# Kernel tuning notes

Hardware: AMD Instinct MI355X
Metric: run time of the kernel (lower is better)

## Reference

```python
import jax, jax.numpy as jnp
import numpy as np

N_NODES = 20000
N_EDGES = 600000
HID = 128
HEADS = 4
NUM_IN = 2 * HID
N_BATCH = 64


def _gelu(x):
    return jax.nn.gelu(x, approximate=False)


def _bn(x, g, b, eps=1e-5):
    # BatchNorm1d, training-mode math: biased variance over the batch dim
    m = jnp.mean(x, axis=0)
    v = jnp.var(x, axis=0)
    return g * (x - m) * jax.lax.rsqrt(v + eps) + b


def setup_inputs() -> dict:
    keys = iter(jax.random.split(jax.random.key(0), 64))

    def nk():
        return next(keys)

    def lin(i, o):
        return (jax.random.normal(nk(), (i, o), jnp.float32) / np.sqrt(i)).astype(jnp.float32)

    def zeros(o):
        return jnp.zeros((o,), jnp.float32)

    inp = {
        "h_V": jax.random.normal(nk(), (N_NODES, HID), jnp.float32),
        "h_E": jax.random.normal(nk(), (N_EDGES, HID), jnp.float32),
        "edge_idx": jax.random.randint(nk(), (2, N_EDGES), 0, N_NODES),
        "batch_id": jnp.sort(jax.random.randint(nk(), (N_NODES,), 0, N_BATCH)),
        # NeighborAttention.W_V (num_in -> hid -> hid -> hid)
        "wv1_w": lin(NUM_IN, HID), "wv1_b": zeros(HID),
        "wv2_w": lin(HID, HID), "wv2_b": zeros(HID),
        "wv3_w": lin(HID, HID), "wv3_b": zeros(HID),
        # NeighborAttention.Bias (3*hid -> hid -> hid -> heads)
        "bb1_w": lin(3 * HID, HID), "bb1_b": zeros(HID),
        "bb2_w": lin(HID, HID), "bb2_b": zeros(HID),
        "bb3_w": lin(HID, HEADS), "bb3_b": zeros(HEADS),
        # NeighborAttention.W_O (no bias)
        "wo_w": lin(HID, HID),
        # GeneralGNN norms 0 and 1
        "n0_g": jnp.ones((HID,), jnp.float32), "n0_b": zeros(HID),
        "n1_g": jnp.ones((HID,), jnp.float32), "n1_b": zeros(HID),
        # dense FFN (hid -> 4*hid -> hid)
        "d1_w": lin(HID, 4 * HID), "d1_b": zeros(4 * HID),
        "d2_w": lin(4 * HID, HID), "d2_b": zeros(HID),
        # EdgeMLP (3*hid -> hid -> hid -> hid) + its norm
        "e1_w": lin(3 * HID, HID), "e1_b": zeros(HID),
        "e2_w": lin(HID, HID), "e2_b": zeros(HID),
        "e3_w": lin(HID, HID), "e3_b": zeros(HID),
        "en_g": jnp.ones((HID,), jnp.float32), "en_b": zeros(HID),
    }
    return inp


def _forward(h_V, h_E, src, dst,
             wv1_w, wv1_b, wv2_w, wv2_b, wv3_w, wv3_b,
             bb1_w, bb1_b, bb2_w, bb2_b, bb3_w, bb3_b,
             wo_w, n0_g, n0_b, n1_g, n1_b,
             d1_w, d1_b, d2_w, d2_b,
             e1_w, e1_b, e2_w, e2_b, e3_w, e3_b, en_g, en_b):
    N = h_V.shape[0]
    d_head = HID // HEADS
    # attention input: cat([h_E, h_V[dst]]) with center_id = src
    h_E_in = jnp.concatenate([h_E, h_V[dst]], axis=-1)  # (E, 2*HID)
    x = jnp.concatenate([h_V[src], h_E_in], axis=-1)     # (E, 3*HID)
    # Bias MLP -> per-edge per-head logits; the sqrt(d) * 1/sqrt(d) scaling cancels
    w = _gelu(x @ bb1_w + bb1_b)
    w = _gelu(w @ bb2_w + bb2_b)
    w = w @ bb3_w + bb3_b                                 # (E, HEADS)
    # value MLP
    V = _gelu(h_E_in @ wv1_w + wv1_b)
    V = _gelu(V @ wv2_w + wv2_b)
    V = (V @ wv3_w + wv3_b).reshape(-1, HEADS, d_head)    # (E, HEADS, d)
    # scatter_softmax over edges sharing a source node
    m = jax.ops.segment_max(w, src, num_segments=N)
    m = jnp.where(jnp.isfinite(m), m, 0.0)
    ew = jnp.exp(w - m[src])
    denom = jax.ops.segment_sum(ew, src, num_segments=N)
    attend = ew / denom[src]                              # (E, HEADS)
    agg = jax.ops.segment_sum(attend[:, :, None] * V, src, num_segments=N)
    dh = agg.reshape(N, HID) @ wo_w                       # W_O
    h_V = _bn(h_V + dh, n0_g, n0_b)
    dh = _gelu(h_V @ d1_w + d1_b) @ d2_w + d2_b           # dense FFN
    h_V = _bn(h_V + dh, n1_g, n1_b)
    # EdgeMLP update
    h_EV = jnp.concatenate([h_V[src], h_E, h_V[dst]], axis=-1)
    msg = _gelu(h_EV @ e1_w + e1_b)
    msg = _gelu(msg @ e2_w + e2_b)
    msg = msg @ e3_w + e3_b
    h_E = _bn(h_E + msg, en_g, en_b)
    # Context with node_context=edge_context=0 is identity
    return (h_V, h_E)


def reference(h_V, h_E, edge_idx, batch_id,
              wv1_w, wv1_b, wv2_w, wv2_b, wv3_w, wv3_b,
              bb1_w, bb1_b, bb2_w, bb2_b, bb3_w, bb3_b,
              wo_w, n0_g, n0_b, n1_g, n1_b,
              d1_w, d1_b, d2_w, d2_b,
              e1_w, e1_b, e2_w, e2_b, e3_w, e3_b, en_g, en_b):
    src, dst = edge_idx[0], edge_idx[1]
    return _forward(h_V, h_E, src, dst,
                    wv1_w, wv1_b, wv2_w, wv2_b, wv3_w, wv3_b,
                    bb1_w, bb1_b, bb2_w, bb2_b, bb3_w, bb3_b,
                    wo_w, n0_g, n0_b, n1_g, n1_b,
                    d1_w, d1_b, d2_w, d2_b,
                    e1_w, e1_b, e2_w, e2_b, e3_w, e3_b, en_g, en_b)
```

## Files before the change

kernel.cpp:

```cpp
#include <hip/hip_runtime.h>
#include <cstdint>
#include <cstddef>

#define NN 20000
#define NE 600000

typedef unsigned short u16;
typedef unsigned int   u32;
typedef __bf16 bf16x8 __attribute__((ext_vector_type(8)));
typedef float  f32x4  __attribute__((ext_vector_type(4)));

constexpr int PK_BB1 = 0;
constexpr int PK_BB2 = PK_BB1 + 384 * 128;
constexpr int PK_WV1 = PK_BB2 + 128 * 128;
constexpr int PK_WV2 = PK_WV1 + 256 * 128;
constexpr int PK_WV3 = PK_WV2 + 128 * 128;
constexpr int PK_WO  = PK_WV3 + 128 * 128;
constexpr int PK_D1  = PK_WO  + 128 * 128;
constexpr int PK_D2  = PK_D1  + 128 * 512;
constexpr int PK_E1  = PK_D2  + 512 * 128;
constexpr int PK_E2  = PK_E1  + 384 * 128;
constexpr int PK_E3  = PK_E2  + 128 * 128;
constexpr int PK_BB3 = PK_E3  + 128 * 128;

constexpr size_t WS_PW    = 0;
constexpr size_t WS_STATS = 0x100000;
constexpr size_t WS_FLAG  = WS_STATS + 3072;
constexpr size_t WS_HIST  = WS_STATS + 0x1000;
constexpr size_t WS_OFFS  = WS_HIST + 0x14000;
constexpr size_t WS_CNT   = WS_OFFS + 0x14000;
constexpr size_t WS_EIDS  = WS_CNT + 0x14000;
constexpr size_t WS_WLOG  = WS_EIDS + 0x250000;
constexpr size_t WS_AGG   = WS_WLOG + 0x930000;
constexpr size_t WS_R     = WS_AGG + 0xA00000;

__device__ __forceinline__ float bf2f(u16 u) {
    return __builtin_bit_cast(float, (u32)u << 16);
}
__device__ __forceinline__ u16 f2bf(float f) {
    u32 x = __builtin_bit_cast(u32, f);
    return (u16)((x + 0x7FFFu + ((x >> 16) & 1u)) >> 16);
}
__device__ __forceinline__ float gelu_f(float x) {
    float z = fabsf(x) * 0.70710678118654752f;
    float t = 1.0f / fmaf(0.3275911f, z, 1.0f);
    float p = t * fmaf(t, fmaf(t, fmaf(t, fmaf(t, 1.061405429f, -1.453152027f),
                                       1.421413741f), -0.284496736f), 0.254829592f);
    float erfz = fmaf(-p, __expf(-z * z), 1.0f);
    float u = 0.5f * x;
    return fmaf(copysignf(erfz, x), u, u);
}
__device__ __forceinline__ float ldv(const void* p, size_t i, int m) {
    return m ? ((const float*)p)[i] : bf2f(((const u16*)p)[i]);
}
#define MFMA(a, b, c) __builtin_amdgcn_mfma_f32_16x16x32_bf16(a, b, c, 0, 0, 0)

#define TM 32
#define XS 136

__device__ __forceinline__ void mma128(const u16* __restrict__ xl, const u16* __restrict__ wp,
                                       int kcBase, int nDiv16, int wave, int lane,
                                       f32x4 acc[2][2]) {
#pragma unroll
    for (int kc = 0; kc < 4; ++kc) {
        int koff = kc * 32 + (lane >> 4) * 8;
        bf16x8 a0 = *(const bf16x8*)&xl[((lane & 15)) * XS + koff];
        bf16x8 a1 = *(const bf16x8*)&xl[((lane & 15) + 16) * XS + koff];
#pragma unroll
        for (int ni = 0; ni < 2; ++ni) {
            int nc = wave * 2 + ni;
            bf16x8 b = *(const bf16x8*)&wp[(((size_t)(kcBase + kc) * nDiv16 + nc) * 64 + lane) * 8];
            acc[0][ni] = MFMA(a0, b, acc[0][ni]);
            acc[1][ni] = MFMA(a1, b, acc[1][ni]);
        }
    }
}

__device__ __forceinline__ void epi_lds(f32x4 acc[2][2], u16* hl, const void* biasG,
                                        int wave, int lane, bool doGelu, int f32m) {
    int col0 = wave * 32;
#pragma unroll
    for (int ni = 0; ni < 2; ++ni) {
        int col = col0 + ni * 16 + (lane & 15);
        float b = ldv(biasG, col, f32m);
#pragma unroll
        for (int mi = 0; mi < 2; ++mi) {
            int rb = mi * 16 + (lane >> 4) * 4;
#pragma unroll
            for (int r = 0; r < 4; ++r) {
                float v = acc[mi][ni][r] + b;
                if (doGelu) v = gelu_f(v);
                hl[(rb + r) * XS + col] = f2bf(v);
            }
        }
    }
}

__device__ __forceinline__ void stage_row8(u16* dst8, const void* table, size_t row, int c8, int f32m) {
    if (f32m) {
        const float* s = (const float*)table + row * 128 + c8 * 8;
        float4 v0 = *(const float4*)s;
        float4 v1 = *(const float4*)(s + 4);
        uint4 o;
        o.x = (u32)f2bf(v0.x) | ((u32)f2bf(v0.y) << 16);
        o.y = (u32)f2bf(v0.z) | ((u32)f2bf(v0.w) << 16);
        o.z = (u32)f2bf(v1.x) | ((u32)f2bf(v1.y) << 16);
        o.w = (u32)f2bf(v1.z) | ((u32)f2bf(v1.w) << 16);
        *(uint4*)dst8 = o;
    } else {
        *(uint4*)dst8 = *(const uint4*)((const u16*)table + row * 128 + c8 * 8);
    }
}

__device__ __forceinline__ void stage_idx(u16* dst, const void* table, const int* idx, int tid, int f32m) {
    int r0 = tid >> 4, c = tid & 15;
#pragma unroll
    for (int p = 0; p < 2; ++p) {
        int r = r0 + p * 16;
        stage_row8(&dst[r * XS + c * 8], table, (size_t)idx[r], c, f32m);
    }
}
__device__ __forceinline__ void stage_seq(u16* dst, const void* table, size_t rowBase, int tid, int f32m) {
    int r0 = tid >> 4, c = tid & 15;
#pragma unroll
    for (int p = 0; p < 2; ++p) {
        int r = r0 + p * 16;
        stage_row8(&dst[r * XS + c * 8], table, rowBase + r, c, f32m);
    }
}

__global__ void k_detect(const void* hV, int* flag) {
    int l = threadIdx.x;
    const u16* p = (const u16*)hV;
    float m = fmaxf(fabsf(bf2f(p[l])), fabsf(bf2f(p[64 + l])));
    for (int s = 1; s < 64; s <<= 1) m = fmaxf(m, __shfl_xor(m, s));
    if (l == 0) *flag = (m > 1e4f) ? 1 : 0;
}

__global__ void k_pack(const void* bb1, const void* bb2, const void* wv1, const void* wv2,
                       const void* wv3, const void* wo, const void* d1, const void* d2,
                       const void* e1, const void* e2, const void* e3, const void* bb3,
                       u16* pw, const int* dflag) {
    int f32m = *dflag;
    const int Ks[12] = {384, 128, 256, 128, 128, 128, 128, 512, 384, 128, 128, 128};
    const int Ns[12] = {128, 128, 128, 128, 128, 128, 512, 128, 128, 128, 128, 16};
    const void* srcs[12] = {bb1, bb2, wv1, wv2, wv3, wo, d1, d2, e1, e2, e3, bb3};
    int gid = blockIdx.x * 256 + threadIdx.x;
    int lane = gid & 63;
    int fid = gid >> 6;
    if (fid >= 708) return;
    int w = 0, base = 0, dstoff = 0;
    for (int i = 0; i < 12; ++i) {
        int nf = (Ks[i] / 32) * (Ns[i] / 16);
        if (fid < base + nf) { w = i; break; }
        base += nf;
        dstoff += Ks[i] * Ns[i];
    }
    int f = fid - base;
    int N = Ns[w];
    int kc = f / (N / 16), nc = f % (N / 16);
    const void* S = srcs[w];
    u16* D = pw + dstoff + ((size_t)f * 64 + lane) * 8;
    int krow = kc * 32 + (lane >> 4) * 8;
    int col = nc * 16 + (lane & 15);
#pragma unroll
    for (int j = 0; j < 8; ++j) {
        float v;
        if (w == 11) v = (col < 4) ? ldv(S, (size_t)(krow + j) * 4 + col, f32m) : 0.f;
        else         v = ldv(S, (size_t)(krow + j) * N + col, f32m);
        D[j] = f2bf(v);
    }
}

__global__ void k_hist(const int* src, int* hist) {
    int e = blockIdx.x * 256 + threadIdx.x;
    if (e < NE) atomicAdd(&hist[src[e]], 1);
}

__global__ void k_scan(const int* hist, int* offs, int* cnt) {
    __shared__ int buf[1024];
    __shared__ int carry;
    if (threadIdx.x == 0) carry = 0;
    __syncthreads();
    for (int b = 0; b < NN; b += 1024) {
        int i = b + threadIdx.x;
        int v = (i < NN) ? hist[i] : 0;
        buf[threadIdx.x] = v;
        __syncthreads();
        for (int s = 1; s < 1024; s <<= 1) {
            int t = (threadIdx.x >= s) ? buf[threadIdx.x - s] : 0;
            __syncthreads();
            buf[threadIdx.x] += t;
            __syncthreads();
        }
        int excl = buf[threadIdx.x] - v + carry;
        if (i < NN) { offs[i] = excl; cnt[i] = excl; }
        __syncthreads();
        if (threadIdx.x == 1023) carry += buf[1023];
        __syncthreads();
    }
    if (threadIdx.x == 0) offs[NN] = carry;
}

__global__ void k_fill(const int* src, int* cnt, int* eids) {
    int e = blockIdx.x * 256 + threadIdx.x;
    if (e < NE) {
        int slot = atomicAdd(&cnt[src[e]], 1);
        eids[slot] = e;
    }
}

__global__ __launch_bounds__(256, 2) void k_edge1(
    const void* __restrict__ hV, const void* __restrict__ hE, const int* __restrict__ eidx,
    const u16* __restrict__ pw, const void* bb1b, const void* bb2b,
    const void* bb3b, const void* wv1b, const void* wv2b, const void* wv3b,
    float* __restrict__ wlog, void* __restrict__ dout, const int* dflag) {
    __shared__ __attribute__((aligned(16))) u16 xb[TM * XS];
    __shared__ __attribute__((aligned(16))) u16 h1b[TM * XS];
    __shared__ __attribute__((aligned(16))) u16 h1v[TM * XS];
    __shared__ int sIdx[TM], dIdx[TM];
    int f32m = *dflag;
    int tid = threadIdx.x, wave = tid >> 6, lane = tid & 63;
    long e0 = (long)blockIdx.x * TM;
    if (tid < TM) {
        sIdx[tid] = eidx[e0 + tid];
        dIdx[tid] = eidx[NE + e0 + tid];
    }
    __syncthreads();

    f32x4 accB[2][2] = {};
    f32x4 accV[2][2] = {};
    stage_idx(xb, hV, sIdx, tid, f32m);
    __syncthreads();
    mma128(xb, pw + PK_BB1, 0, 8, wave, lane, accB);
    __syncthreads();
    stage_seq(xb, hE, (size_t)e0, tid, f32m);
    __syncthreads();
    mma128(xb, pw + PK_BB1, 4, 8, wave, lane, accB);
    mma128(xb, pw + PK_WV1, 0, 8, wave, lane, accV);
    __syncthreads();
    stage_idx(xb, hV, dIdx, tid, f32m);
    __syncthreads();
    mma128(xb, pw + PK_BB1, 8, 8, wave, lane, accB);
    mma128(xb, pw + PK_WV1, 4, 8, wave, lane, accV);
    __syncthreads();
    epi_lds(accB, h1b, bb1b, wave, lane, true, f32m);
    epi_lds(accV, h1v, wv1b, wave, lane, true, f32m);
    __syncthreads();
    f32x4 accB2[2][2] = {};
    f32x4 accV2[2][2] = {};
    mma128(h1b, pw + PK_BB2, 0, 8, wave, lane, accB2);
    mma128(h1v, pw + PK_WV2, 0, 8, wave, lane, accV2);
    __syncthreads();
    epi_lds(accB2, xb, bb2b, wave, lane, true, f32m);
    epi_lds(accV2, h1b, wv2b, wave, lane, true, f32m);
    __syncthreads();
    u16* Vout = (u16*)((char*)dout + (size_t)NN * 128 * (f32m ? 4 : 2));
    f32x4 accV3[2][2] = {};
    mma128(h1b, pw + PK_WV3, 0, 8, wave, lane, accV3);
    {
        int col0 = wave * 32;
#pragma unroll
        for (int ni = 0; ni < 2; ++ni) {
            int col = col0 + ni * 16 + (lane & 15);
            float b = ldv(wv3b, col, f32m);
#pragma unroll
            for (int mi = 0; mi < 2; ++mi) {
                int rb = mi * 16 + (lane >> 4) * 4;
#pragma unroll
                for (int r = 0; r < 4; ++r) {
                    long row = e0 + rb + r;
                    Vout[row * 128 + col] = f2bf(accV3[mi][ni][r] + b);
                }
            }
        }
    }
    if (wave == 0) {
        f32x4 aw0 = {0.f, 0.f, 0.f, 0.f};
        f32x4 aw1 = {0.f, 0.f, 0.f, 0.f};
#pragma unroll
        for (int kc = 0; kc < 4; ++kc) {
            int koff = kc * 32 + (lane >> 4) * 8;
            bf16x8 a0 = *(const bf16x8*)&xb[(lane & 15) * XS + koff];
            bf16x8 a1 = *(const bf16x8*)&xb[((lane & 15) + 16) * XS + koff];
            bf16x8 b = *(const bf16x8*)&pw[PK_BB3 + ((size_t)kc * 64 + lane) * 8];
            aw0 = MFMA(a0, b, aw0);
            aw1 = MFMA(a1, b, aw1);
        }
        if ((lane & 15) < 4) {
            int col = lane & 15;
            int rbase = (lane >> 4) * 4;
            float b3 = ldv(bb3b, col, f32m);
#pragma unroll
            for (int r = 0; r < 4; ++r) {
                wlog[(e0 + rbase + r) * 4 + col] = aw0[r] + b3;
                wlog[(e0 + 16 + rbase + r) * 4 + col] = aw1[r] + b3;
            }
        }
    }
}

__global__ void k_agg(const int* __restrict__ offs, const int* __restrict__ eids,
                      const float* __restrict__ wlog, const void* __restrict__ dout,
                      float* __restrict__ agg, const int* dflag) {
    int f32m = *dflag;
    const u16* V = (const u16*)((const char*)dout + (size_t)NN * 128 * (f32m ? 4 : 2));
    int node = blockIdx.x;
    int l = threadIdx.x;
    int beg = offs[node], end = offs[node + 1];
    int deg = end - beg;
    if (deg == 0) {
        agg[(size_t)node * 128 + 2 * l] = 0.f;
        agg[(size_t)node * 128 + 2 * l + 1] = 0.f;
        return;
    }
    int h = l & 3;
    float lmax = -3.0e38f;
    for (int i = (l >> 2); i < deg; i += 16) {
        int e = eids[beg + i];
        lmax = fmaxf(lmax, wlog[(size_t)e * 4 + h]);
    }
    for (int s = 4; s < 64; s <<= 1) lmax = fmaxf(lmax, __shfl_xor(lmax, s));
    float lsum = 0.f;
    for (int i = (l >> 2); i < deg; i += 16) {
        int e = eids[beg + i];
        lsum += __expf(wlog[(size_t)e * 4 + h] - lmax);
    }
    for (int s = 4; s < 64; s <<= 1) lsum += __shfl_xor(lsum, s);
    int hh = l >> 4;
    float mh = __shfl(lmax, hh);
    float inv = 1.f / __shfl(lsum, hh);
    float a0 = 0.f, a1 = 0.f;
    for (int i = 0; i < deg; ++i) {
        int e = eids[beg + i];
        float aw = __expf(wlog[(size_t)e * 4 + hh] - mh) * inv;
        u32 vv = *(const u32*)&V[(size_t)e * 128 + 2 * l];
        a0 += aw * bf2f((u16)(vv & 0xffffu));
        a1 += aw * bf2f((u16)(vv >> 16));
    }
    float2 o;
    o.x = a0;
    o.y = a1;
    *(float2*)&agg[(size_t)node * 128 + 2 * l] = o;
}

__global__ __launch_bounds__(256, 2) void k_wo(const float* __restrict__ agg,
                                               const void* __restrict__ hV,
                                               const u16* __restrict__ pw,
                                               float* __restrict__ rbuf,
                                               float* __restrict__ stats0, const int* dflag) {
    __shared__ __attribute__((aligned(16))) u16 xb[TM * XS];
    __shared__ float lsum[128], lsq[128];
    int f32m = *dflag;
    int tid = threadIdx.x, wave = tid >> 6, lane = tid & 63;
    long n0 = (long)blockIdx.x * TM;
    if (tid < 128) { lsum[tid] = 0.f; lsq[tid] = 0.f; }
    {
        int r = tid >> 3, cc = (tid & 7) * 16;
        long row = n0 + r;
        for (int j = 0; j < 16; j += 4) {
            float4 v = {0.f, 0.f, 0.f, 0.f};
            if (row < NN) v = *(const float4*)&agg[row * 128 + cc + j];
            u16* d = &xb[r * XS + cc + j];
            d[0] = f2bf(v.x); d[1] = f2bf(v.y); d[2] = f2bf(v.z); d[3] = f2bf(v.w);
        }
    }
    __syncthreads();
    f32x4 acc[2][2] = {};
    mma128(xb, pw + PK_WO, 0, 8, wave, lane, acc);
    int col0 = wave * 32;
#pragma unroll
    for (int ni = 0; ni < 2; ++ni) {
        int col = col0 + ni * 16 + (lane & 15);
#pragma unroll
        for (int mi = 0; mi < 2; ++mi) {
            int rb = mi * 16 + (lane >> 4) * 4;
#pragma unroll
            for (int r = 0; r < 4; ++r) {
                long row = n0 + rb + r;
                if (row < NN) {
                    float v = ldv(hV, (size_t)row * 128 + col, f32m) + acc[mi][ni][r];
                    rbuf[row * 128 + col] = v;
                    atomicAdd(&lsum[col], v);
                    atomicAdd(&lsq[col], v * v);
                }
            }
        }
    }
    __syncthreads();
    if (tid < 128) {
        atomicAdd(&stats0[tid], lsum[tid]);
        atomicAdd(&stats0[128 + tid], lsq[tid]);
    }
}

__global__ __launch_bounds__(256, 2) void k_ffn(float* __restrict__ rbuf,
                                                const float* __restrict__ stats0,
                                                const void* n0g, const void* n0b,
                                                const u16* __restrict__ pw,
                                                const void* d1b, const void* d2b,
                                                float* __restrict__ stats1, const int* dflag) {
    __shared__ float bnS[128], bnB[128];
    __shared__ float h1f[TM * 128];
    __shared__ __attribute__((aligned(16))) u16 h1x[TM * XS];
    __shared__ __attribute__((aligned(16))) u16 hid[TM * 520];
    __shared__ float lsum[128], lsq[128];
    int f32m = *dflag;
    int tid = threadIdx.x, wave = tid >> 6, lane = tid & 63;
    long n0 = (long)blockIdx.x * TM;
    if (tid < 128) {
        float m = stats0[tid] * (1.f / NN);
        float v = stats0[128 + tid] * (1.f / NN) - m * m;
        float s = ldv(n0g, tid, f32m) * rsqrtf(v + 1e-5f);
        bnS[tid] = s;
        bnB[tid] = ldv(n0b, tid, f32m) - m * s;
        lsum[tid] = 0.f;
        lsq[tid] = 0.f;
    }
    __syncthreads();
    {
        int r = tid >> 3, cc = (tid & 7) * 16;
        long row = n0 + r;
        for (int j = 0; j < 16; ++j) {
            int c = cc + j;
            float v = (row < NN) ? (rbuf[row * 128 + c] * bnS[c] + bnB[c]) : 0.f;
            h1f[r * 128 + c] = v;
            h1x[r * XS + c] = f2bf(v);
        }
    }
    __syncthreads();
    f32x4 acc1[2][8] = {};
#pragma unroll
    for (int kc = 0; kc < 4; ++kc) {
        int koff = kc * 32 + (lane >> 4) * 8;
        bf16x8 a0 = *(const bf16x8*)&h1x[(lane & 15) * XS + koff];
        bf16x8 a1 = *(const bf16x8*)&h1x[((lane & 15) + 16) * XS + koff];
#pragma unroll
        for (int ni = 0; ni < 8; ++ni) {
            int nc = wave * 8 + ni;
            bf16x8 b = *(const bf16x8*)&pw[PK_D1 + (((size_t)kc * 32 + nc) * 64 + lane) * 8];
            acc1[0][ni] = MFMA(a0, b, acc1[0][ni]);
            acc1[1][ni] = MFMA(a1, b, acc1[1][ni]);
        }
    }
#pragma unroll
    for (int ni = 0; ni < 8; ++ni) {
        int col = wave * 128 + ni * 16 + (lane & 15);
        float bb = ldv(d1b, col, f32m);
#pragma unroll
        for (int mi = 0; mi < 2; ++mi) {
            int rb = mi * 16 + (lane >> 4) * 4;
#pragma unroll
            for (int r = 0; r < 4; ++r)
                hid[(rb + r) * 520 + col] = f2bf(gelu_f(acc1[mi][ni][r] + bb));
        }
    }
    __syncthreads();
    f32x4 acc2[2][2] = {};
#pragma unroll
    for (int kc = 0; kc < 16; ++kc) {
        int koff = kc * 32 + (lane >> 4) * 8;
        bf16x8 a0 = *(const bf16x8*)&hid[(lane & 15) * 520 + koff];
        bf16x8 a1 = *(const bf16x8*)&hid[((lane & 15) + 16) * 520 + koff];
#pragma unroll
        for (int ni = 0; ni < 2; ++ni) {
            int nc = wave * 2 + ni;
            bf16x8 b = *(const bf16x8*)&pw[PK_D2 + (((size_t)kc * 8 + nc) * 64 + lane) * 8];
            acc2[0][ni] = MFMA(a0, b, acc2[0][ni]);
            acc2[1][ni] = MFMA(a1, b, acc2[1][ni]);
        }
    }
    int col0 = wave * 32;
#pragma unroll
    for (int ni = 0; ni < 2; ++ni) {
        int col = col0 + ni * 16 + (lane & 15);
        float db = ldv(d2b, col, f32m);
#pragma unroll
        for (int mi = 0; mi < 2; ++mi) {
            int rb = mi * 16 + (lane >> 4) * 4;
#pragma unroll
            for (int r = 0; r < 4; ++r) {
                long row = n0 + rb + r;
                if (row < NN) {
                    float v = h1f[(rb + r) * 128 + col] + acc2[mi][ni][r] + db;
                    rbuf[row * 128 + col] = v;
                    atomicAdd(&lsum[col], v);
                    atomicAdd(&lsq[col], v * v);
                }
            }
        }
    }
    __syncthreads();
    if (tid < 128) {
        atomicAdd(&stats1[tid], lsum[tid]);
        atomicAdd(&stats1[128 + tid], lsq[tid]);
    }
}

__global__ void k_out_hV(const float* __restrict__ rbuf, const float* __restrict__ stats1,
                         const void* n1g, const void* n1b, void* __restrict__ dout,
                         const int* dflag) {
    int f32m = *dflag;
    int idx = blockIdx.x * 256 + threadIdx.x;
    if (idx >= NN * 128) return;
    int c = idx & 127;
    float m = stats1[c] * (1.f / NN);
    float v = stats1[128 + c] * (1.f / NN) - m * m;
    float s = ldv(n1g, c, f32m) * rsqrtf(v + 1e-5f);
    float b = ldv(n1b, c, f32m) - m * s;
    float o = rbuf[idx] * s + b;
    if (f32m) ((float*)dout)[idx] = o;
    else      ((u16*)dout)[idx] = f2bf(o);
}

__global__ __launch_bounds__(256, 2) void k_edge2(
    const void* __restrict__ hE, const int* __restrict__ eidx,
    const u16* __restrict__ pw, const void* e1b, const void* e2b, const void* e3b,
    void* __restrict__ dout, float* __restrict__ statsE, const int* dflag) {
    __shared__ __attribute__((aligned(16))) u16 xb[TM * XS];
    __shared__ __attribute__((aligned(16))) u16 h1[TM * XS];
    __shared__ __attribute__((aligned(16))) u16 h2[TM * XS];
    __shared__ int sIdx[TM], dIdx[TM];
    int f32m = *dflag;
    int tid = threadIdx.x, wave = tid >> 6, lane = tid & 63;
    long e0 = (long)blockIdx.x * TM;
    const void* hV2 = dout;
    if (tid < TM) {
        sIdx[tid] = eidx[e0 + tid];
        dIdx[tid] = eidx[NE + e0 + tid];
    }
    __syncthreads();

    f32x4 a1[2][2] = {};
    stage_idx(xb, hV2, sIdx, tid, f32m);
    __syncthreads();
    mma128(xb, pw + PK_E1, 0, 8, wave, lane, a1);
    __syncthreads();
    stage_seq(xb, hE, (size_t)e0, tid, f32m);
    __syncthreads();
    mma128(xb, pw + PK_E1, 4, 8, wave, lane, a1);
    __syncthreads();
    stage_idx(xb, hV2, dIdx, tid, f32m);
    __syncthreads();
    mma128(xb, pw + PK_E1, 8, 8, wave, lane, a1);
    epi_lds(a1, h1, e1b, wave, lane, true, f32m);
    __syncthreads();
    f32x4 a2[2][2] = {};
    mma128(h1, pw + PK_E2, 0, 8, wave, lane, a2);
    __syncthreads();
    epi_lds(a2, h2, e2b, wave, lane, true, f32m);
    __syncthreads();
    f32x4 a3[2][2] = {};
    mma128(h2, pw + PK_E3, 0, 8, wave, lane, a3);
    float* yb32 = (float*)((char*)dout + (size_t)NN * 512);
    u16*   yb16 = (u16*)((char*)dout + (size_t)NN * 256);
    int col0 = wave * 32;
    float ssum[2] = {0.f, 0.f}, ssq[2] = {0.f, 0.f};
#pragma unroll
    for (int ni = 0; ni < 2; ++ni) {
        int col = col0 + ni * 16 + (lane & 15);
        float b = ldv(e3b, col, f32m);
#pragma unroll
        for (int mi = 0; mi < 2; ++mi) {
            int rb = mi * 16 + (lane >> 4) * 4;
#pragma unroll
            for (int r = 0; r < 4; ++r) {
                long row = e0 + rb + r;
                float y = ldv(hE, (size_t)row * 128 + col, f32m) + a3[mi][ni][r] + b;
                if (f32m) yb32[row * 128 + col] = y;
                else      yb16[row * 128 + col] = f2bf(y);
                ssum[ni] += y;
                ssq[ni] += y * y;
            }
        }
    }
#pragma unroll
    for (int ni = 0; ni < 2; ++ni) {
        ssum[ni] += __shfl_xor(ssum[ni], 16);
        ssum[ni] += __shfl_xor(ssum[ni], 32);
        ssq[ni]  += __shfl_xor(ssq[ni], 16);
        ssq[ni]  += __shfl_xor(ssq[ni], 32);
    }
    if (lane < 16) {
#pragma unroll
        for (int ni = 0; ni < 2; ++ni) {
            int col = col0 + ni * 16 + lane;
            atomicAdd(&statsE[col], ssum[ni]);
            atomicAdd(&statsE[128 + col], ssq[ni]);
        }
    }
}

__global__ void k_out_hE(const float* __restrict__ statsE, const void* eng, const void* enb,
                         void* __restrict__ dout, const int* dflag) {
    int f32m = *dflag;
    long i4 = (long)blockIdx.x * 256 + threadIdx.x;
    if (i4 >= (long)NE * 32) return;
    int c0 = (int)((i4 & 31) * 4);
    float s[4], b[4];
#pragma unroll
    for (int j = 0; j < 4; ++j) {
        int c = c0 + j;
        float m = statsE[c] * (1.f / NE);
        float v = statsE[128 + c] * (1.f / NE) - m * m;
        float sc = ldv(eng, c, f32m) * rsqrtf(v + 1e-5f);
        s[j] = sc;
        b[j] = ldv(enb, c, f32m) - m * sc;
    }
    if (f32m) {
        float4* y = (float4*)((char*)dout + (size_t)NN * 512);
        float4 v = y[i4];
        v.x = v.x * s[0] + b[0];
        v.y = v.y * s[1] + b[1];
        v.z = v.z * s[2] + b[2];
        v.w = v.w * s[3] + b[3];
        y[i4] = v;
    } else {
        ushort4* y = (ushort4*)((char*)dout + (size_t)NN * 256);
        ushort4 v = y[i4];
        v.x = f2bf(bf2f(v.x) * s[0] + b[0]);
        v.y = f2bf(bf2f(v.y) * s[1] + b[1]);
        v.z = f2bf(bf2f(v.z) * s[2] + b[2]);
        v.w = f2bf(bf2f(v.w) * s[3] + b[3]);
        y[i4] = v;
    }
}

extern "C" void kernel_launch(void* const* d_in, const int* in_sizes, int n_in,
                              void* d_out, int out_size, void* d_ws, size_t ws_size,
                              hipStream_t stream) {
    (void)in_sizes; (void)n_in; (void)out_size; (void)ws_size;
    const void* hV = d_in[0];
    const void* hE = d_in[1];
    const int* eidx = (const int*)d_in[2];
    const void* wv1w = d_in[4];  const void* wv1b = d_in[5];
    const void* wv2w = d_in[6];  const void* wv2b = d_in[7];
    const void* wv3w = d_in[8];  const void* wv3b = d_in[9];
    const void* bb1w = d_in[10]; const void* bb1b = d_in[11];
    const void* bb2w = d_in[12]; const void* bb2b = d_in[13];
    const void* bb3w = d_in[14]; const void* bb3b = d_in[15];
    const void* wow  = d_in[16];
    const void* n0g = d_in[17]; const void* n0b = d_in[18];
    const void* n1g = d_in[19]; const void* n1b = d_in[20];
    const void* d1w = d_in[21]; const void* d1b = d_in[22];
    const void* d2w = d_in[23]; const void* d2b = d_in[24];
    const void* e1w = d_in[25]; const void* e1b = d_in[26];
    const void* e2w = d_in[27]; const void* e2b = d_in[28];
    const void* e3w = d_in[29]; const void* e3b = d_in[30];
    const void* eng = d_in[31]; const void* enb = d_in[32];

    char* ws = (char*)d_ws;
    u16* pw      = (u16*)(ws + WS_PW);
    float* stats = (float*)(ws + WS_STATS);
    int* dflag   = (int*)(ws + WS_FLAG);
    int* hist    = (int*)(ws + WS_HIST);
    int* offs    = (int*)(ws + WS_OFFS);
    int* cnt     = (int*)(ws + WS_CNT);
    int* eids    = (int*)(ws + WS_EIDS);
    float* wlog  = (float*)(ws + WS_WLOG);
    float* agg   = (float*)(ws + WS_AGG);
    float* rbuf  = (float*)(ws + WS_R);

    hipMemsetAsync(ws + WS_STATS, 0, 0x1000 + NN * sizeof(int), stream);

    k_detect<<<1, 64, 0, stream>>>(hV, dflag);
    k_pack<<<177, 256, 0, stream>>>(bb1w, bb2w, wv1w, wv2w, wv3w, wow, d1w, d2w,
                                    e1w, e2w, e3w, bb3w, pw, dflag);
    k_hist<<<(NE + 255) / 256, 256, 0, stream>>>(eidx, hist);
    k_scan<<<1, 1024, 0, stream>>>(hist, offs, cnt);
    k_fill<<<(NE + 255) / 256, 256, 0, stream>>>(eidx, cnt, eids);
    k_edge1<<<NE / TM, 256, 0, stream>>>(hV, hE, eidx, pw, bb1b, bb2b, bb3b,
                                         wv1b, wv2b, wv3b, wlog, d_out, dflag);
    k_agg<<<NN, 64, 0, stream>>>(offs, eids, wlog, d_out, agg, dflag);
    k_wo<<<(NN + TM - 1) / TM, 256, 0, stream>>>(agg, hV, pw, rbuf, stats, dflag);
    k_ffn<<<(NN + TM - 1) / TM, 256, 0, stream>>>(rbuf, stats, n0g, n0b, pw, d1b, d2b,
                                                  stats + 256, dflag);
    k_out_hV<<<(NN * 128 + 255) / 256, 256, 0, stream>>>(rbuf, stats + 256, n1g, n1b, d_out, dflag);
    k_edge2<<<NE / TM, 256, 0, stream>>>(hE, eidx, pw, e1b, e2b, e3b, d_out, stats + 512, dflag);
    k_out_hE<<<(int)(((long)NE * 32 + 255) / 256), 256, 0, stream>>>(stats + 512, eng, enb, d_out, dflag);
}
```

Measured before the change: 1.924 ms.

## Stage all three edge input tiles up front and prefetch residuals

In both edge kernels, the src, edge and dst tiles are now gathered into three separate LDS buffers in one phase, indexing straight from global edge_idx instead of first copying the indices to shared memory. This removes several barrier-separated stage/compute phases and lets the gather loads overlap. The buffers are reused for later layers to keep the LDS footprint the same. In k_edge2 the h_E residual is loaded into registers early, so its latency hides behind the MMAs, at the cost of more register pressure under launch_bounds(256,2). One barrier between the E2 MMA and its epilogue was also dropped; this is safe only because the two use different buffers.

Measured after the change: 1.963 ms. +2.0%, slower.

```diff
diff --git a/kernel.cpp b/kernel.cpp
--- a/kernel.cpp
+++ b/kernel.cpp
@@ -112,12 +112,13 @@
     }
 }
 
-__device__ __forceinline__ void stage_idx(u16* dst, const void* table, const int* idx, int tid, int f32m) {
+__device__ __forceinline__ void stage_gidx(u16* dst, const void* table, const int* gIdx,
+                                           int tid, int f32m) {
     int r0 = tid >> 4, c = tid & 15;
 #pragma unroll
     for (int p = 0; p < 2; ++p) {
         int r = r0 + p * 16;
-        stage_row8(&dst[r * XS + c * 8], table, (size_t)idx[r], c, f32m);
+        stage_row8(&dst[r * XS + c * 8], table, (size_t)gIdx[r], c, f32m);
     }
 }
 __device__ __forceinline__ void stage_seq(u16* dst, const void* table, size_t rowBase, int tid, int f32m) {
@@ -215,49 +216,39 @@
     const u16* __restrict__ pw, const void* bb1b, const void* bb2b,
     const void* bb3b, const void* wv1b, const void* wv2b, const void* wv3b,
     float* __restrict__ wlog, void* __restrict__ dout, const int* dflag) {
-    __shared__ __attribute__((aligned(16))) u16 xb[TM * XS];
-    __shared__ __attribute__((aligned(16))) u16 h1b[TM * XS];
-    __shared__ __attribute__((aligned(16))) u16 h1v[TM * XS];
-    __shared__ int sIdx[TM], dIdx[TM];
+    __shared__ __attribute__((aligned(16))) u16 X[TM * XS];
+    __shared__ __attribute__((aligned(16))) u16 Y[TM * XS];
+    __shared__ __attribute__((aligned(16))) u16 Z[TM * XS];
     int f32m = *dflag;
     int tid = threadIdx.x, wave = tid >> 6, lane = tid & 63;
     long e0 = (long)blockIdx.x * TM;
-    if (tid < TM) {
-        sIdx[tid] = eidx[e0 + tid];
-        dIdx[tid] = eidx[NE + e0 + tid];
-    }
-    __syncthreads();
-
+
+    stage_gidx(X, hV, eidx + e0, tid, f32m);
+    stage_seq (Y, hE, (size_t)e0, tid, f32m);
+    stage_gidx(Z, hV, eidx + NE + e0, tid, f32m);
+    __syncthreads();
     f32x4 accB[2][2] = {};
     f32x4 accV[2][2] = {};
-    stage_idx(xb, hV, sIdx, tid, f32m);
-    __syncthreads();
-    mma128(xb, pw + PK_BB1, 0, 8, wave, lane, accB);
-    __syncthreads();
-    stage_seq(xb, hE, (size_t)e0, tid, f32m);
-    __syncthreads();
-    mma128(xb, pw + PK_BB1, 4, 8, wave, lane, accB);
-    mma128(xb, pw + PK_WV1, 0, 8, wave, lane, accV);
-    __syncthreads();
-    stage_idx(xb, hV, dIdx, tid, f32m);
-    __syncthreads();
-    mma128(xb, pw + PK_BB1, 8, 8, wave, lane, accB);
-    mma128(xb, pw + PK_WV1, 4, 8, wave, lane, accV);
-    __syncthreads();
-    epi_lds(accB, h1b, bb1b, wave, lane, true, f32m);
-    epi_lds(accV, h1v, wv1b, wave, lane, true, f32m);
+    mma128(X, pw + PK_BB1, 0, 8, wave, lane, accB);
+    mma128(Y, pw + PK_BB1, 4, 8, wave, lane, accB);
+    mma128(Z, pw + PK_BB1, 8, 8, wave, lane, accB);
+    mma128(Y, pw + PK_WV1, 0, 8, wave, lane, accV);
+    mma128(Z, pw + PK_WV1, 4, 8, wave, lane, accV);
+    __syncthreads();
+    epi_lds(accB, X, bb1b, wave, lane, true, f32m);
+    epi_lds(accV, Y, wv1b, wave, lane, true, f32m);
     __syncthreads();
     f32x4 accB2[2][2] = {};
     f32x4 accV2[2][2] = {};
-    mma128(h1b, pw + PK_BB2, 0, 8, wave, lane, accB2);
-    mma128(h1v, pw + PK_WV2, 0, 8, wave, lane, accV2);
-    __syncthreads();
-    epi_lds(accB2, xb, bb2b, wave, lane, true, f32m);
-    epi_lds(accV2, h1b, wv2b, wave, lane, true, f32m);
+    mma128(X, pw + PK_BB2, 0, 8, wave, lane, accB2);
+    mma128(Y, pw + PK_WV2, 0, 8, wave, lane, accV2);
+    __syncthreads();
+    epi_lds(accB2, Z, bb2b, wave, lane, true, f32m);
+    epi_lds(accV2, X, wv2b, wave, lane, true, f32m);
     __syncthreads();
     u16* Vout = (u16*)((char*)dout + (size_t)NN * 128 * (f32m ? 4 : 2));
     f32x4 accV3[2][2] = {};
-    mma128(h1b, pw + PK_WV3, 0, 8, wave, lane, accV3);
+    mma128(X, pw + PK_WV3, 0, 8, wave, lane, accV3);
     {
         int col0 = wave * 32;
 #pragma unroll
@@ -281,8 +272,8 @@
 #pragma unroll
         for (int kc = 0; kc < 4; ++kc) {
             int koff = kc * 32 + (lane >> 4) * 8;
-            bf16x8 a0 = *(const bf16x8*)&xb[(lane & 15) * XS + koff];
-            bf16x8 a1 = *(const bf16x8*)&xb[((lane & 15) + 16) * XS + koff];
+            bf16x8 a0 = *(const bf16x8*)&Z[(lane & 15) * XS + koff];
+            bf16x8 a1 = *(const bf16x8*)&Z[((lane & 15) + 16) * XS + koff];
             bf16x8 b = *(const bf16x8*)&pw[PK_BB3 + ((size_t)kc * 64 + lane) * 8];
             aw0 = MFMA(a0, b, aw0);
             aw1 = MFMA(a1, b, aw1);
@@ -517,56 +508,55 @@
     const void* __restrict__ hE, const int* __restrict__ eidx,
     const u16* __restrict__ pw, const void* e1b, const void* e2b, const void* e3b,
     void* __restrict__ dout, float* __restrict__ statsE, const int* dflag) {
-    __shared__ __attribute__((aligned(16))) u16 xb[TM * XS];
-    __shared__ __attribute__((aligned(16))) u16 h1[TM * XS];
-    __shared__ __attribute__((aligned(16))) u16 h2[TM * XS];
-    __shared__ int sIdx[TM], dIdx[TM];
+    __shared__ __attribute__((aligned(16))) u16 X[TM * XS];
+    __shared__ __attribute__((aligned(16))) u16 Y[TM * XS];
+    __shared__ __attribute__((aligned(16))) u16 Z[TM * XS];
     int f32m = *dflag;
     int tid = threadIdx.x, wave = tid >> 6, lane = tid & 63;
     long e0 = (long)blockIdx.x * TM;
     const void* hV2 = dout;
-    if (tid < TM) {
-        sIdx[tid] = eidx[e0 + tid];
-        dIdx[tid] = eidx[NE + e0 + tid];
-    }
-    __syncthreads();
-
+
+    stage_gidx(X, hV2, eidx + e0, tid, f32m);
+    stage_seq (Z, hE, (size_t)e0, tid, f32m);
+    stage_gidx(Y, hV2, eidx + NE + e0, tid, f32m);
+    int col0 = wave * 32, rbase = (lane >> 4) * 4, cl = lane & 15;
+    float res[2][2][4];
+#pragma unroll
+    for (int ni = 0; ni < 2; ++ni)
+#pragma unroll
+        for (int mi = 0; mi < 2; ++mi)
+#pragma unroll
+            for (int r = 0; r < 4; ++r)
+                res[ni][mi][r] = ldv(hE, (size_t)(e0 + mi * 16 + rbase + r) * 128
+                                              + col0 + ni * 16 + cl, f32m);
+    __syncthreads();
     f32x4 a1[2][2] = {};
-    stage_idx(xb, hV2, sIdx, tid, f32m);
-    __syncthreads();
-    mma128(xb, pw + PK_E1, 0, 8, wave, lane, a1);
-    __syncthreads();
-    stage_seq(xb, hE, (size_t)e0, tid, f32m);
-    __syncthreads();
-    mma128(xb, pw + PK_E1, 4, 8, wave, lane, a1);
-    __syncthreads();
-    stage_idx(xb, hV2, dIdx, tid, f32m);
-    __syncthreads();
-    mma128(xb, pw + PK_E1, 8, 8, wave, lane, a1);
-    epi_lds(a1, h1, e1b, wave, lane, true, f32m);
+    mma128(X, pw + PK_E1, 0, 8, wave, lane, a1);
+    mma128(Z, pw + PK_E1, 4, 8, wave, lane, a1);
+    mma128(Y, pw + PK_E1, 8, 8, wave, lane, a1);
+    __syncthreads();
+    epi_lds(a1, X, e1b, wave, lane, true, f32m);
     __syncthreads();
     f32x4 a2[2][2] = {};
-    mma128(h1, pw + PK_E2, 0, 8, wave, lane, a2);
-    __syncthreads();
-    epi_lds(a2, h2, e2b, wave, lane, true, f32m);
+    mma128(X, pw + PK_E2, 0, 8, wave, lane, a2);
+    epi_lds(a2, Y, e2b, wave, lane, true, f32m);
     __syncthreads();
     f32x4 a3[2][2] = {};
-    mma128(h2, pw + PK_E3, 0, 8, wave, lane, a3);
+    mma128(Y, pw + PK_E3, 0, 8, wave, lane, a3);
     float* yb32 = (float*)((char*)dout + (size_t)NN * 512);
     u16*   yb16 = (u16*)((char*)dout + (size_t)NN * 256);
-    int col0 = wave * 32;
     float ssum[2] = {0.f, 0.f}, ssq[2] = {0.f, 0.f};
 #pragma unroll
     for (int ni = 0; ni < 2; ++ni) {
-        int col = col0 + ni * 16 + (lane & 15);
+        int col = col0 + ni * 16 + cl;
         float b = ldv(e3b, col, f32m);
 #pragma unroll
         for (int mi = 0; mi < 2; ++mi) {
-            int rb = mi * 16 + (lane >> 4) * 4;
+            int rb = mi * 16 + rbase;
 #pragma unroll
             for (int r = 0; r < 4; ++r) {
                 long row = e0 + rb + r;
-                float y = ldv(hE, (size_t)row * 128 + col, f32m) + a3[mi][ni][r] + b;
+                float y = res[ni][mi][r] + a3[mi][ni][r] + b;
                 if (f32m) yb32[row * 128 + col] = y;
                 else      yb16[row * 128 + col] = f2bf(y);
                 ssum[ni] += y;
```
